# Optimization experiments

Hardware: AMD Instinct MI355X
Metric: run time of the kernel (lower is better)

## Reference

```python
import jax, jax.numpy as jnp
import numpy as np

B, T, C = 2, 2048, 1024
N_HEAD = 16
HEAD_DIM = C // N_HEAD
ROPE_BASE = 10000.0


def setup_inputs() -> dict:
    key = jax.random.key(0)
    ks = jax.random.split(key, 5)
    s = 0.02
    return {
        "x": jax.random.normal(ks[0], (B, T, C), dtype=jnp.float32),
        "Wq": jax.random.normal(ks[1], (C, C), dtype=jnp.float32) * s,
        "Wk": jax.random.normal(ks[2], (C, C), dtype=jnp.float32) * s,
        "Wv": jax.random.normal(ks[3], (C, C), dtype=jnp.float32) * s,
        "Wo": jax.random.normal(ks[4], (C, C), dtype=jnp.float32) * s,
    }


def _rope_cos_sin(seq_len, head_dim, dtype):
    inv_freq = 1.0 / (ROPE_BASE ** (jnp.arange(0, head_dim, 2, dtype=jnp.float32) / head_dim))
    t = jnp.arange(seq_len, dtype=jnp.float32)
    freqs = jnp.einsum("i,j->ij", t, inv_freq)          # [T, head_dim/2]
    emb = jnp.concatenate([freqs, freqs], axis=-1)        # [T, head_dim]
    return jnp.cos(emb).astype(dtype), jnp.sin(emb).astype(dtype)


def _rotate_half(x):
    x1, x2 = jnp.split(x, 2, axis=-1)
    return jnp.concatenate([-x2, x1], axis=-1)


def _mha(x, Wq, Wk, Wv, Wo):
    b, t, c = x.shape
    # torch nn.Linear stores weight [out, in]: y = x @ W.T
    q = (x @ Wq.T).reshape(b, t, N_HEAD, HEAD_DIM).transpose(0, 2, 1, 3)  # [B,H,T,D]
    k = (x @ Wk.T).reshape(b, t, N_HEAD, HEAD_DIM).transpose(0, 2, 1, 3)
    v = (x @ Wv.T).reshape(b, t, N_HEAD, HEAD_DIM).transpose(0, 2, 1, 3)
    cos, sin = _rope_cos_sin(t, HEAD_DIM, x.dtype)        # [T,D] each, broadcast over B,H
    q = q * cos + _rotate_half(q) * sin
    k = k * cos + _rotate_half(k) * sin
    scale = 1.0 / np.sqrt(HEAD_DIM).astype(np.float32)
    att = jnp.einsum("bhqd,bhkd->bhqk", q, k) * scale     # [B,H,T,T]
    causal = jnp.tril(jnp.ones((t, t), dtype=bool))
    att = jnp.where(causal, att, jnp.finfo(att.dtype).min)
    att = jax.nn.softmax(att, axis=-1)
    y = jnp.einsum("bhqk,bhkd->bhqd", att, v)             # [B,H,T,D]
    y = y.transpose(0, 2, 1, 3).reshape(b, t, c)
    return y @ Wo.T


def reference(x, Wq, Wk, Wv, Wo):
    return _mha(x, Wq, Wk, Wv, Wo)
```

## Files before the change

kernel.cpp:

```cpp
#include <hip/hip_runtime.h>

#define BB 2
#define TT 2048
#define CC 1024
#define NH 16
#define HD 64

typedef __attribute__((ext_vector_type(8))) short bf16x8;
typedef __attribute__((ext_vector_type(4))) float floatx4;
typedef __attribute__((ext_vector_type(16))) float floatx16;

__device__ __forceinline__ unsigned short f2bf(float f) {
    union { float f; unsigned int u; } v; v.f = f;
    unsigned int u = v.u;
    u = (u + 0x7fffu + ((u >> 16) & 1u)) >> 16;
    return (unsigned short)u;
}

typedef __attribute__((address_space(3))) unsigned char* lds_ptr_t;
typedef const __attribute__((address_space(1))) unsigned char* glob_ptr_t;
__device__ __forceinline__ void gll16(const void* g, void* l) {
    __builtin_amdgcn_global_load_lds((glob_ptr_t)g, (lds_ptr_t)l, 16, 0, 0);
}

__global__ __launch_bounds__(256) void cast_all_k(const float* __restrict__ x,
                                                  const float* __restrict__ wq,
                                                  const float* __restrict__ wk,
                                                  const float* __restrict__ wv,
                                                  const float* __restrict__ wo,
                                                  unsigned short* __restrict__ xb,
                                                  unsigned short* __restrict__ wqkvb,
                                                  unsigned short* __restrict__ wob) {
    int i = blockIdx.x * 256 + threadIdx.x;
    const float* src;
    unsigned short* dst;
    if (i < 1048576) {
        src = x + (size_t)i * 4;
        dst = xb + (size_t)i * 4;
    } else {
        int w   = (i - 1048576) >> 18;
        int off = (i - 1048576) & 262143;
        const float* s0 = (w == 0) ? wq : (w == 1) ? wk : (w == 2) ? wv : wo;
        unsigned short* d0 = (w == 3) ? wob : (wqkvb + (size_t)w * 1048576);
        src = s0 + (size_t)off * 4;
        dst = d0 + (size_t)off * 4;
    }
    float4 v = *(const float4*)src;
    ushort4 o;
    o.x = f2bf(v.x); o.y = f2bf(v.y); o.z = f2bf(v.z); o.w = f2bf(v.w);
    *(ushort4*)dst = o;
}

__global__ __launch_bounds__(256) void gemm128_k(const unsigned short* __restrict__ A,
                                                 const unsigned short* __restrict__ Bt,
                                                 float* __restrict__ C, int M, int N, int K) {
    __shared__ __align__(16) unsigned short As[128][32];
    __shared__ __align__(16) unsigned short Bs[128][32];
    const int tid  = threadIdx.x;
    const int wave = tid >> 6;
    const int lane = tid & 63;
    const int quad = lane >> 4;
    const int l16  = lane & 15;
    const int wr = (wave >> 1) * 64;
    const int wc = (wave & 1) * 64;
    const int row0 = blockIdx.y * 128;
    const int col0 = blockIdx.x * 128;
    const int srow = tid >> 2;
    const int scol = (tid & 3) * 8;

    const unsigned short* Ap0 = A  + (size_t)(row0 + srow) * K + scol;
    const unsigned short* Ap1 = A  + (size_t)(row0 + 64 + srow) * K + scol;
    const unsigned short* Bp0 = Bt + (size_t)(col0 + srow) * K + scol;
    const unsigned short* Bp1 = Bt + (size_t)(col0 + 64 + srow) * K + scol;

    floatx4 acc[4][4];
    #pragma unroll
    for (int i = 0; i < 4; i++)
        #pragma unroll
        for (int j = 0; j < 4; j++) acc[i][j] = (floatx4){0.f, 0.f, 0.f, 0.f};

    for (int k0 = 0; k0 < K; k0 += 32) {
        __syncthreads();
        gll16(Ap0 + k0, &As[srow][scol]);
        gll16(Ap1 + k0, &As[64 + srow][scol]);
        gll16(Bp0 + k0, &Bs[srow][scol]);
        gll16(Bp1 + k0, &Bs[64 + srow][scol]);
        __syncthreads();
        bf16x8 af[4], bfr[4];
        #pragma unroll
        for (int i = 0; i < 4; i++) af[i]  = *(const bf16x8*)&As[wr + 16 * i + l16][quad * 8];
        #pragma unroll
        for (int j = 0; j < 4; j++) bfr[j] = *(const bf16x8*)&Bs[wc + 16 * j + l16][quad * 8];
        #pragma unroll
        for (int i = 0; i < 4; i++)
            #pragma unroll
            for (int j = 0; j < 4; j++)
                acc[i][j] = __builtin_amdgcn_mfma_f32_16x16x32_bf16(af[i], bfr[j], acc[i][j], 0, 0, 0);
    }

    #pragma unroll
    for (int i = 0; i < 4; i++)
        #pragma unroll
        for (int j = 0; j < 4; j++)
            #pragma unroll
            for (int r = 0; r < 4; r++) {
                int row = row0 + wr + 16 * i + quad * 4 + r;
                int col = col0 + wc + 16 * j + l16;
                C[(size_t)row * N + col] = acc[i][j][r];
            }
}

__global__ __launch_bounds__(256) void gemm_qkv_k(const unsigned short* __restrict__ A,
                                                  const unsigned short* __restrict__ Bt,
                                                  unsigned short* __restrict__ Qb,
                                                  unsigned short* __restrict__ Kb,
                                                  unsigned short* __restrict__ Vb) {
    __shared__ __align__(16) unsigned short As[128][32];
    __shared__ __align__(16) unsigned short Bs[128][32];
    const int K = 1024;
    const int tid  = threadIdx.x;
    const int wave = tid >> 6;
    const int lane = tid & 63;
    const int quad = lane >> 4;
    const int l16  = lane & 15;
    const int wr = (wave >> 1) * 64;
    const int wc = (wave & 1) * 64;
    const int row0 = blockIdx.y * 128;
    const int col0 = blockIdx.x * 128;
    const int srow = tid >> 2;
    const int scol = (tid & 3) * 8;

    const unsigned short* Ap0 = A  + (size_t)(row0 + srow) * K + scol;
    const unsigned short* Ap1 = A  + (size_t)(row0 + 64 + srow) * K + scol;
    const unsigned short* Bp0 = Bt + (size_t)(col0 + srow) * K + scol;
    const unsigned short* Bp1 = Bt + (size_t)(col0 + 64 + srow) * K + scol;

    floatx4 acc[4][4];
    #pragma unroll
    for (int i = 0; i < 4; i++)
        #pragma unroll
        for (int j = 0; j < 4; j++) acc[i][j] = (floatx4){0.f, 0.f, 0.f, 0.f};

    for (int k0 = 0; k0 < K; k0 += 32) {
        __syncthreads();
        gll16(Ap0 + k0, &As[srow][scol]);
        gll16(Ap1 + k0, &As[64 + srow][scol]);
        gll16(Bp0 + k0, &Bs[srow][scol]);
        gll16(Bp1 + k0, &Bs[64 + srow][scol]);
        __syncthreads();
        bf16x8 af[4], bfr[4];
        #pragma unroll
        for (int i = 0; i < 4; i++) af[i]  = *(const bf16x8*)&As[wr + 16 * i + l16][quad * 8];
        #pragma unroll
        for (int j = 0; j < 4; j++) bfr[j] = *(const bf16x8*)&Bs[wc + 16 * j + l16][quad * 8];
        #pragma unroll
        for (int i = 0; i < 4; i++)
            #pragma unroll
            for (int j = 0; j < 4; j++)
                acc[i][j] = __builtin_amdgcn_mfma_f32_16x16x32_bf16(af[i], bfr[j], acc[i][j], 0, 0, 0);
    }

    const int colw = col0 + wc;
    const int sect = colw >> 10;
    const int h    = (colw & 1023) >> 6;

    if (sect == 2) {
        #pragma unroll
        for (int i = 0; i < 4; i++)
            #pragma unroll
            for (int r = 0; r < 4; r++) {
                int row = row0 + wr + 16 * i + quad * 4 + r;
                int t = row & (TT - 1);
                size_t base = ((size_t)((row >> 11) * NH + h) * TT + t) * 64;
                #pragma unroll
                for (int j = 0; j < 4; j++)
                    Vb[base + 16 * j + l16] = f2bf(acc[i][j][r]);
            }
    } else {
        unsigned short* dst = sect ? Kb : Qb;
        const float qs = sect ? 1.0f : 0.18033688011112f;
        const float C1 = 0.41524101186092f;
        const float I2PI = 0.15915494309189535f;
        float invf0 = __builtin_amdgcn_exp2f(-(float)l16 * C1) * I2PI;
        float invf1 = __builtin_amdgcn_exp2f(-(float)(16 + l16) * C1) * I2PI;
        #pragma unroll
        for (int i = 0; i < 4; i++) {
            #pragma unroll
            for (int r = 0; r < 4; r++) {
                int row = row0 + wr + 16 * i + quad * 4 + r;
                int t = row & (TT - 1);
                size_t base = ((size_t)((row >> 11) * NH + h) * TT + t) * 64;
                #pragma unroll
                for (int jj = 0; jj < 2; jj++) {
                    float rev = (float)t * (jj ? invf1 : invf0);
                    rev -= floorf(rev);
                    float ang = rev * 6.2831853071796f;
                    float c = __cosf(ang), s = __sinf(ang);
                    float v1 = acc[i][jj][r], v2 = acc[i][jj + 2][r];
                    dst[base + 16 * jj + l16]      = f2bf((v1 * c - v2 * s) * qs);
                    dst[base + 16 * jj + 32 + l16] = f2bf((v2 * c + v1 * s) * qs);
                }
            }
        }
    }
}

__global__ __launch_bounds__(256) void vtr_k(const unsigned short* __restrict__ Vb,
                                             unsigned short* __restrict__ Vt) {
    __shared__ __align__(16) unsigned short Vsh[64][70];
    const int tid = threadIdx.x;
    const int tt = blockIdx.x;
    const int bh = blockIdx.y;
    const int sr = tid >> 2;
    const int sc = (tid & 3) * 16;
    const unsigned short* src = Vb + ((size_t)bh * TT + tt * 64 + sr) * 64 + sc;
    *(int4*)&Vsh[sr][sc]     = *(const int4*)src;
    *(int4*)&Vsh[sr][sc + 8] = *(const int4*)(src + 8);
    __syncthreads();
    const int dr = tid >> 2;
    const int tc = (tid & 3) * 16;
    unsigned short tv[16];
    #pragma unroll
    for (int i = 0; i < 16; i++) {
        int x = tc + i;
        int key = (x & ~15) + (x & 3) + ((x >> 2) & 1) * 8 + ((x >> 3) & 1) * 4;
        tv[i] = Vsh[key][dr];
    }
    size_t vo = ((size_t)bh * 64 + dr) * TT + tt * 64 + tc;
    *(int4*)(Vt + vo)     = *(int4*)&tv[0];
    *(int4*)(Vt + vo + 8) = *(int4*)&tv[8];
}

__global__ __launch_bounds__(256, 4) void flash_k(const unsigned short* __restrict__ Qb,
                                                  const unsigned short* __restrict__ Kb,
                                                  const unsigned short* __restrict__ Vt,
                                                  float* __restrict__ O0, float* __restrict__ O1,
                                                  float* __restrict__ L0, float* __restrict__ L1) {
    __shared__ __align__(16) unsigned short Ks[64][72];
    __shared__ __align__(16) unsigned short Vs[64][72];
    const int tid  = threadIdx.x;
    const int wave = tid >> 6;
    const int lane = tid & 63;
    const int h    = lane >> 5;
    const int l32  = lane & 31;
    const int qt    = 15 - (blockIdx.x >> 6);
    const int inner = blockIdx.x & 63;
    const int bh    = inner >> 1;
    const int split = inner & 1;
    const int q0 = qt * 128;
    const int qw = q0 + wave * 32 + l32;
    const int sr = tid >> 2;
    const int sc = (tid & 3) * 16;

    bf16x8 qf[4];
    {
        const unsigned short* qp = Qb + ((size_t)bh * TT + qw) * 64 + h * 8;
        #pragma unroll
        for (int kk = 0; kk < 4; kk++) qf[kk] = *(const bf16x8*)(qp + kk * 16);
    }

    floatx16 accO[2];
    accO[0] = (floatx16)(0.f);
    accO[1] = (floatx16)(0.f);
    float lsum = 0.f;

    const int kt0 = split * (qt + 1);
    const int kt1 = kt0 + qt + 1;
    const unsigned short* kbase = Kb + (size_t)bh * TT * 64;
    const unsigned short* vbase = Vt + (size_t)bh * 64 * TT;

    const unsigned short* kp = kbase + ((size_t)(kt0 * 64) + sr) * 64 + sc;
    const unsigned short* vp = vbase + (size_t)sr * TT + kt0 * 64 + sc;
    int4 ka = *(const int4*)kp, kb2 = *(const int4*)(kp + 8);
    int4 va = *(const int4*)vp, vb2 = *(const int4*)(vp + 8);

    for (int kt = kt0; kt < kt1; kt++) {
        __syncthreads();
        *(int4*)&Ks[sr][sc]     = ka;
        *(int4*)&Ks[sr][sc + 8] = kb2;
        *(int4*)&Vs[sr][sc]     = va;
        *(int4*)&Vs[sr][sc + 8] = vb2;
        __syncthreads();
        if (kt + 1 < kt1) {
            const unsigned short* kp2 = kbase + ((size_t)((kt + 1) * 64) + sr) * 64 + sc;
            const unsigned short* vp2 = vbase + (size_t)sr * TT + (kt + 1) * 64 + sc;
            ka  = *(const int4*)kp2; kb2 = *(const int4*)(kp2 + 8);
            va  = *(const int4*)vp2; vb2 = *(const int4*)(vp2 + 8);
        }

        const bool diag = (kt >= 2 * qt);
        bf16x8 pfrag[4];

        #pragma unroll
        for (int mb = 0; mb < 2; mb++) {
            floatx16 sacc = (floatx16)(0.f);
            #pragma unroll
            for (int kk = 0; kk < 4; kk++) {
                bf16x8 kf = *(const bf16x8*)&Ks[32 * mb + l32][kk * 16 + h * 8];
                sacc = __builtin_amdgcn_mfma_f32_32x32x16_bf16(kf, qf[kk], sacc, 0, 0, 0);
            }
            float p[16];
            const int kmb = kt * 64 + 32 * mb + 4 * h;
            #pragma unroll
            for (int r = 0; r < 16; r++) {
                float pv = __builtin_amdgcn_exp2f(sacc[r]);
                if (diag) {
                    int ki = kmb + (r & 3) + 8 * (r >> 2);
                    if (ki > qw) pv = 0.f;
                }
                lsum += pv;
                p[r] = pv;
            }
            #pragma unroll
            for (int half = 0; half < 2; half++) {
                union { bf16x8 v; unsigned u[4]; } pk;
                #pragma unroll
                for (int i = 0; i < 4; i++) {
                    unsigned ulo = __float_as_uint(p[half * 8 + 2 * i]);
                    unsigned uhi = __float_as_uint(p[half * 8 + 2 * i + 1]);
                    pk.u[i] = (ulo >> 16) | (uhi & 0xffff0000u);
                }
                pfrag[2 * mb + half] = pk.v;
            }
        }

        #pragma unroll
        for (int mbo = 0; mbo < 2; mbo++) {
            #pragma unroll
            for (int kk = 0; kk < 4; kk++) {
                bf16x8 vf = *(const bf16x8*)&Vs[32 * mbo + l32][kk * 16 + h * 8];
                accO[mbo] = __builtin_amdgcn_mfma_f32_32x32x16_bf16(vf, pfrag[kk], accO[mbo], 0, 0, 0);
            }
        }
    }

    lsum += __shfl_xor(lsum, 32);
    float* Op = split ? O1 : O0;
    float* Lp = split ? L1 : L0;
    if (lane < 32) Lp[(size_t)bh * TT + qw] = lsum;
    float* orow = Op + ((size_t)bh * TT + qw) * 64;
    #pragma unroll
    for (int mbo = 0; mbo < 2; mbo++)
        #pragma unroll
        for (int a = 0; a < 4; a++) {
            float4 o4;
            o4.x = accO[mbo][4 * a + 0];
            o4.y = accO[mbo][4 * a + 1];
            o4.z = accO[mbo][4 * a + 2];
            o4.w = accO[mbo][4 * a + 3];
            *(float4*)(orow + 32 * mbo + 8 * a + 4 * h) = o4;
        }
}

__global__ __launch_bounds__(256) void combine_k(const float* __restrict__ O0,
                                                 const float* __restrict__ O1,
                                                 const float* __restrict__ L0,
                                                 const float* __restrict__ L1,
                                                 unsigned short* __restrict__ Yb) {
    int idx = blockIdx.x * 256 + threadIdx.x;
    int dg  = idx & 15;
    int row = idx >> 4;
    float inv = 1.0f / (L0[row] + L1[row]);
    float4 a = ((const float4*)O0)[idx];
    float4 b = ((const float4*)O1)[idx];
    ushort4 o;
    o.x = f2bf((a.x + b.x) * inv);
    o.y = f2bf((a.y + b.y) * inv);
    o.z = f2bf((a.z + b.z) * inv);
    o.w = f2bf((a.w + b.w) * inv);
    int bh = row >> 11, t = row & (TT - 1);
    int bb = bh >> 4, h = bh & 15;
    *(ushort4*)(Yb + ((size_t)(bb * TT + t)) * CC + h * 64 + dg * 4) = o;
}

extern "C" void kernel_launch(void* const* d_in, const int* in_sizes, int n_in,
                              void* d_out, int out_size, void* d_ws, size_t ws_size,
                              hipStream_t stream) {
    (void)in_sizes; (void)n_in; (void)out_size; (void)ws_size;
    const float* x  = (const float*)d_in[0];
    const float* Wq = (const float*)d_in[1];
    const float* Wk = (const float*)d_in[2];
    const float* Wv = (const float*)d_in[3];
    const float* Wo = (const float*)d_in[4];
    float* out = (float*)d_out;
    char* ws = (char*)d_ws;

    unsigned short* xb    = (unsigned short*)(ws + 0);
    unsigned short* wqkvb = (unsigned short*)(ws + (8ull  << 20));
    unsigned short* wob   = (unsigned short*)(ws + (14ull << 20));
    unsigned short* Qb    = (unsigned short*)(ws + (16ull << 20));
    unsigned short* Kb    = (unsigned short*)(ws + (24ull << 20));
    unsigned short* Vb    = (unsigned short*)(ws + (32ull << 20));
    unsigned short* Vt    = (unsigned short*)(ws + (40ull << 20));
    unsigned short* Yb    = (unsigned short*)(ws + (48ull << 20));
    float* O0 = (float*)(ws + (56ull << 20));
    float* O1 = (float*)(ws + (72ull << 20));
    float* L0 = (float*)(ws + (88ull << 20));
    float* L1 = (float*)(ws + (88ull << 20) + (256ull << 10));

    cast_all_k<<<8192, 256, 0, stream>>>(x, Wq, Wk, Wv, Wo, xb, wqkvb, wob);
    gemm_qkv_k<<<dim3(24, 32), 256, 0, stream>>>(xb, wqkvb, Qb, Kb, Vb);
    vtr_k<<<dim3(32, 32), 256, 0, stream>>>(Vb, Vt);
    flash_k<<<1024, 256, 0, stream>>>(Qb, Kb, Vt, O0, O1, L0, L1);
    combine_k<<<4096, 256, 0, stream>>>(O0, O1, L0, L1, Yb);
    gemm128_k<<<dim3(8, 32), 256, 0, stream>>>(Yb, wob, out, 4096, 1024, 1024);
}
```

Baseline: 202.2 us.

## Stage QKV epilogue through LDS, precompute RoPE table, bf16 partials, XCD-aware tiling

The QKV GEMM epilogue now writes its accumulators to swizzled LDS and re-reads them row-wise, so Q/K/V are stored with 16-byte vector writes. RoPE cos/sin values, with the Q scale folded in, come from a table that extra blocks of the cast kernel build. The flash partial outputs O0/O1 are stored as bf16 instead of fp32, halving combine traffic at some precision cost. Both GEMMs remap block indices so that blocks on the same XCD share row tiles, aiming for better L2 reuse.

Result: faster. 192.0 us (-5.1%).

```diff
diff --git a/kernel.cpp b/kernel.cpp
--- a/kernel.cpp
+++ b/kernel.cpp
@@ -15,6 +15,9 @@
     unsigned int u = v.u;
     u = (u + 0x7fffu + ((u >> 16) & 1u)) >> 16;
     return (unsigned short)u;
+}
+__device__ __forceinline__ float bf2f(unsigned short u) {
+    return __uint_as_float((unsigned)u << 16);
 }
 
 typedef __attribute__((address_space(3))) unsigned char* lds_ptr_t;
@@ -30,7 +33,23 @@
                                                   const float* __restrict__ wo,
                                                   unsigned short* __restrict__ xb,
                                                   unsigned short* __restrict__ wqkvb,
-                                                  unsigned short* __restrict__ wob) {
+                                                  unsigned short* __restrict__ wob,
+                                                  float2* __restrict__ tabQ,
+                                                  float2* __restrict__ tabK) {
+    if (blockIdx.x >= 8192) {
+        int idx = (blockIdx.x - 8192) * 256 + threadIdx.x;
+        int t = idx >> 5, j = idx & 31;
+        const float C1 = 0.41524101186092f;
+        const float I2PI = 0.15915494309189535f;
+        float rev = (float)t * (__builtin_amdgcn_exp2f(-(float)j * C1) * I2PI);
+        rev -= floorf(rev);
+        float ang = rev * 6.2831853071796f;
+        float c = __cosf(ang), s = __sinf(ang);
+        const float qs = 0.18033688011112f;
+        tabK[idx] = make_float2(c, s);
+        tabQ[idx] = make_float2(c * qs, s * qs);
+        return;
+    }
     int i = blockIdx.x * 256 + threadIdx.x;
     const float* src;
     unsigned short* dst;
@@ -53,7 +72,7 @@
 
 __global__ __launch_bounds__(256) void gemm128_k(const unsigned short* __restrict__ A,
                                                  const unsigned short* __restrict__ Bt,
-                                                 float* __restrict__ C, int M, int N, int K) {
+                                                 float* __restrict__ C, int N, int K) {
     __shared__ __align__(16) unsigned short As[128][32];
     __shared__ __align__(16) unsigned short Bs[128][32];
     const int tid  = threadIdx.x;
@@ -63,8 +82,10 @@
     const int l16  = lane & 15;
     const int wr = (wave >> 1) * 64;
     const int wc = (wave & 1) * 64;
-    const int row0 = blockIdx.y * 128;
-    const int col0 = blockIdx.x * 128;
+    const int bid = blockIdx.x;
+    const int xcd = bid & 7, sl = bid >> 3;
+    const int row0 = (xcd * 4 + (sl >> 3)) * 128;
+    const int col0 = (sl & 7) * 128;
     const int srow = tid >> 2;
     const int scol = (tid & 3) * 8;
 
@@ -112,11 +133,15 @@
 
 __global__ __launch_bounds__(256) void gemm_qkv_k(const unsigned short* __restrict__ A,
                                                   const unsigned short* __restrict__ Bt,
+                                                  const float2* __restrict__ tabQ,
+                                                  const float2* __restrict__ tabK,
                                                   unsigned short* __restrict__ Qb,
                                                   unsigned short* __restrict__ Kb,
                                                   unsigned short* __restrict__ Vb) {
-    __shared__ __align__(16) unsigned short As[128][32];
-    __shared__ __align__(16) unsigned short Bs[128][32];
+    __shared__ __align__(16) unsigned short SMEM[128 * 128];
+    unsigned short (*As)[32] = (unsigned short(*)[32])SMEM;
+    unsigned short (*Bs)[32] = (unsigned short(*)[32])(SMEM + 128 * 32);
+    unsigned short (*Eb)[128] = (unsigned short(*)[128])SMEM;
     const int K = 1024;
     const int tid  = threadIdx.x;
     const int wave = tid >> 6;
@@ -125,8 +150,10 @@
     const int l16  = lane & 15;
     const int wr = (wave >> 1) * 64;
     const int wc = (wave & 1) * 64;
-    const int row0 = blockIdx.y * 128;
-    const int col0 = blockIdx.x * 128;
+    const int bid = blockIdx.x;
+    const int xcd = bid & 7, sl = bid >> 3;
+    const int row0 = (xcd * 4 + sl / 24) * 128;
+    const int col0 = (sl % 24) * 128;
     const int srow = tid >> 2;
     const int scol = (tid & 3) * 8;
 
@@ -160,48 +187,54 @@
                 acc[i][j] = __builtin_amdgcn_mfma_f32_16x16x32_bf16(af[i], bfr[j], acc[i][j], 0, 0, 0);
     }
 
-    const int colw = col0 + wc;
-    const int sect = colw >> 10;
-    const int h    = (colw & 1023) >> 6;
-
+    __syncthreads();
+    #pragma unroll
+    for (int i = 0; i < 4; i++)
+        #pragma unroll
+        for (int j = 0; j < 4; j++)
+            #pragma unroll
+            for (int r = 0; r < 4; r++) {
+                int erow = wr + 16 * i + quad * 4 + r;
+                int col  = wc + 16 * j + l16;
+                int pcol = (((col >> 3) ^ (erow & 15)) << 3) | (col & 7);
+                Eb[erow][pcol] = f2bf(acc[i][j][r]);
+            }
+    __syncthreads();
+
+    const int row  = tid >> 1;
+    const int half = tid & 1;
+    const int grow = row0 + row;
+    const int t    = grow & (TT - 1);
+    const int bb   = grow >> 11;
+    const int sect = col0 >> 10;
+    const int hh   = ((col0 & 1023) >> 6) + half;
+    union { int4 q[8]; unsigned short u[64]; } raw;
+    #pragma unroll
+    for (int i = 0; i < 8; i++) {
+        int pg = (half * 8 + i) ^ (row & 15);
+        raw.q[i] = *(const int4*)&Eb[row][pg << 3];
+    }
+    size_t obase = ((size_t)(bb * NH + hh) * TT + t) * 64;
     if (sect == 2) {
         #pragma unroll
-        for (int i = 0; i < 4; i++)
-            #pragma unroll
-            for (int r = 0; r < 4; r++) {
-                int row = row0 + wr + 16 * i + quad * 4 + r;
-                int t = row & (TT - 1);
-                size_t base = ((size_t)((row >> 11) * NH + h) * TT + t) * 64;
-                #pragma unroll
-                for (int j = 0; j < 4; j++)
-                    Vb[base + 16 * j + l16] = f2bf(acc[i][j][r]);
-            }
+        for (int i = 0; i < 8; i++) *(int4*)(Vb + obase + 8 * i) = raw.q[i];
     } else {
+        const float4* tab = (const float4*)((sect ? tabK : tabQ) + (size_t)t * 32);
         unsigned short* dst = sect ? Kb : Qb;
-        const float qs = sect ? 1.0f : 0.18033688011112f;
-        const float C1 = 0.41524101186092f;
-        const float I2PI = 0.15915494309189535f;
-        float invf0 = __builtin_amdgcn_exp2f(-(float)l16 * C1) * I2PI;
-        float invf1 = __builtin_amdgcn_exp2f(-(float)(16 + l16) * C1) * I2PI;
-        #pragma unroll
-        for (int i = 0; i < 4; i++) {
-            #pragma unroll
-            for (int r = 0; r < 4; r++) {
-                int row = row0 + wr + 16 * i + quad * 4 + r;
-                int t = row & (TT - 1);
-                size_t base = ((size_t)((row >> 11) * NH + h) * TT + t) * 64;
-                #pragma unroll
-                for (int jj = 0; jj < 2; jj++) {
-                    float rev = (float)t * (jj ? invf1 : invf0);
-                    rev -= floorf(rev);
-                    float ang = rev * 6.2831853071796f;
-                    float c = __cosf(ang), s = __sinf(ang);
-                    float v1 = acc[i][jj][r], v2 = acc[i][jj + 2][r];
-                    dst[base + 16 * jj + l16]      = f2bf((v1 * c - v2 * s) * qs);
-                    dst[base + 16 * jj + 32 + l16] = f2bf((v2 * c + v1 * s) * qs);
-                }
-            }
+        union { int4 q[8]; unsigned short u[64]; } o;
+        #pragma unroll
+        for (int i = 0; i < 16; i++) {
+            float4 cs = tab[i];
+            int j0 = 2 * i, j1 = 2 * i + 1;
+            float a0 = bf2f(raw.u[j0]), b0 = bf2f(raw.u[j0 + 32]);
+            float a1 = bf2f(raw.u[j1]), b1 = bf2f(raw.u[j1 + 32]);
+            o.u[j0]      = f2bf(a0 * cs.x - b0 * cs.y);
+            o.u[j0 + 32] = f2bf(b0 * cs.x + a0 * cs.y);
+            o.u[j1]      = f2bf(a1 * cs.z - b1 * cs.w);
+            o.u[j1 + 32] = f2bf(b1 * cs.z + a1 * cs.w);
         }
+        #pragma unroll
+        for (int i = 0; i < 8; i++) *(int4*)(dst + obase + 8 * i) = o.q[i];
     }
 }
 
@@ -234,7 +267,8 @@
 __global__ __launch_bounds__(256, 4) void flash_k(const unsigned short* __restrict__ Qb,
                                                   const unsigned short* __restrict__ Kb,
                                                   const unsigned short* __restrict__ Vt,
-                                                  float* __restrict__ O0, float* __restrict__ O1,
+                                                  unsigned short* __restrict__ O0,
+                                                  unsigned short* __restrict__ O1,
                                                   float* __restrict__ L0, float* __restrict__ L1) {
     __shared__ __align__(16) unsigned short Ks[64][72];
     __shared__ __align__(16) unsigned short Vs[64][72];
@@ -335,25 +369,25 @@
     }
 
     lsum += __shfl_xor(lsum, 32);
-    float* Op = split ? O1 : O0;
+    unsigned short* Op = split ? O1 : O0;
     float* Lp = split ? L1 : L0;
     if (lane < 32) Lp[(size_t)bh * TT + qw] = lsum;
-    float* orow = Op + ((size_t)bh * TT + qw) * 64;
+    unsigned short* orow = Op + ((size_t)bh * TT + qw) * 64;
     #pragma unroll
     for (int mbo = 0; mbo < 2; mbo++)
         #pragma unroll
         for (int a = 0; a < 4; a++) {
-            float4 o4;
-            o4.x = accO[mbo][4 * a + 0];
-            o4.y = accO[mbo][4 * a + 1];
-            o4.z = accO[mbo][4 * a + 2];
-            o4.w = accO[mbo][4 * a + 3];
-            *(float4*)(orow + 32 * mbo + 8 * a + 4 * h) = o4;
+            ushort4 o4;
+            o4.x = f2bf(accO[mbo][4 * a + 0]);
+            o4.y = f2bf(accO[mbo][4 * a + 1]);
+            o4.z = f2bf(accO[mbo][4 * a + 2]);
+            o4.w = f2bf(accO[mbo][4 * a + 3]);
+            *(ushort4*)(orow + 32 * mbo + 8 * a + 4 * h) = o4;
         }
 }
 
-__global__ __launch_bounds__(256) void combine_k(const float* __restrict__ O0,
-                                                 const float* __restrict__ O1,
+__global__ __launch_bounds__(256) void combine_k(const unsigned short* __restrict__ O0,
+                                                 const unsigned short* __restrict__ O1,
                                                  const float* __restrict__ L0,
                                                  const float* __restrict__ L1,
                                                  unsigned short* __restrict__ Yb) {
@@ -361,16 +395,20 @@
     int dg  = idx & 15;
     int row = idx >> 4;
     float inv = 1.0f / (L0[row] + L1[row]);
-    float4 a = ((const float4*)O0)[idx];
-    float4 b = ((const float4*)O1)[idx];
+    uint2 a = ((const uint2*)O0)[idx];
+    uint2 b = ((const uint2*)O1)[idx];
+    float a0 = __uint_as_float(a.x << 16),      b0 = __uint_as_float(b.x << 16);
+    float a1 = __uint_as_float(a.x & 0xffff0000u), b1 = __uint_as_float(b.x & 0xffff0000u);
+    float a2 = __uint_as_float(a.y << 16),      b2 = __uint_as_float(b.y << 16);
+    float a3 = __uint_as_float(a.y & 0xffff0000u), b3 = __uint_as_float(b.y & 0xffff0000u);
     ushort4 o;
-    o.x = f2bf((a.x + b.x) * inv);
-    o.y = f2bf((a.y + b.y) * inv);
-    o.z = f2bf((a.z + b.z) * inv);
-    o.w = f2bf((a.w + b.w) * inv);
+    o.x = f2bf((a0 + b0) * inv);
+    o.y = f2bf((a1 + b1) * inv);
+    o.z = f2bf((a2 + b2) * inv);
+    o.w = f2bf((a3 + b3) * inv);
     int bh = row >> 11, t = row & (TT - 1);
-    int bb = bh >> 4, h = bh & 15;
-    *(ushort4*)(Yb + ((size_t)(bb * TT + t)) * CC + h * 64 + dg * 4) = o;
+    int bb = bh >> 4, hh = bh & 15;
+    *(ushort4*)(Yb + ((size_t)(bb * TT + t)) * CC + hh * 64 + dg * 4) = o;
 }
 
 extern "C" void kernel_launch(void* const* d_in, const int* in_sizes, int n_in,
@@ -393,15 +431,17 @@
     unsigned short* Vb    = (unsigned short*)(ws + (32ull << 20));
     unsigned short* Vt    = (unsigned short*)(ws + (40ull << 20));
     unsigned short* Yb    = (unsigned short*)(ws + (48ull << 20));
-    float* O0 = (float*)(ws + (56ull << 20));
-    float* O1 = (float*)(ws + (72ull << 20));
-    float* L0 = (float*)(ws + (88ull << 20));
-    float* L1 = (float*)(ws + (88ull << 20) + (256ull << 10));
-
-    cast_all_k<<<8192, 256, 0, stream>>>(x, Wq, Wk, Wv, Wo, xb, wqkvb, wob);
-    gemm_qkv_k<<<dim3(24, 32), 256, 0, stream>>>(xb, wqkvb, Qb, Kb, Vb);
+    unsigned short* O0    = (unsigned short*)(ws + (56ull << 20));
+    unsigned short* O1    = (unsigned short*)(ws + (64ull << 20));
+    float* L0 = (float*)(ws + (72ull << 20));
+    float* L1 = (float*)(ws + (72ull << 20) + (256ull << 10));
+    float2* tabQ = (float2*)(ws + (73ull << 20));
+    float2* tabK = (float2*)(ws + (73ull << 20) + (512ull << 10));
+
+    cast_all_k<<<8448, 256, 0, stream>>>(x, Wq, Wk, Wv, Wo, xb, wqkvb, wob, tabQ, tabK);
+    gemm_qkv_k<<<768, 256, 0, stream>>>(xb, wqkvb, tabQ, tabK, Qb, Kb, Vb);
     vtr_k<<<dim3(32, 32), 256, 0, stream>>>(Vb, Vt);
     flash_k<<<1024, 256, 0, stream>>>(Qb, Kb, Vt, O0, O1, L0, L1);
     combine_k<<<4096, 256, 0, stream>>>(O0, O1, L0, L1, Yb);
-    gemm128_k<<<dim3(8, 32), 256, 0, stream>>>(Yb, wob, out, 4096, 1024, 1024);
-}
+    gemm128_k<<<256, 256, 0, stream>>>(Yb, wob, out, 1024, 1024);
+}
```
